# Kernel tuning notes

Hardware: AMD Instinct MI355X
Metric: run time of the kernel (lower is better)

## Reference

```python
import jax, jax.numpy as jnp
import numpy as np

B, T = 128, 512
V, E, U, K = 50000, 100, 128, 32


def _lstm(x, Wk, Wr, b):
    # x: [B, T, D] -> [B, T, U], Keras LSTM gate order i,f,g,o
    Bd = x.shape[0]
    Ud = Wr.shape[0]
    xs = jnp.swapaxes(x, 0, 1)  # [T, B, D]

    def step(carry, xt):
        h, c = carry
        z = xt @ Wk + h @ Wr + b
        i, f, g, o = jnp.split(z, 4, axis=-1)
        c = jax.nn.sigmoid(f) * c + jax.nn.sigmoid(i) * jnp.tanh(g)
        h = jax.nn.sigmoid(o) * jnp.tanh(c)
        return (h, c), h

    init = (jnp.zeros((Bd, Ud), x.dtype), jnp.zeros((Bd, Ud), x.dtype))
    _, hs = jax.lax.scan(step, init, xs)
    return jnp.swapaxes(hs, 0, 1)


def _crf_logZ(em, trans):
    # em: [B, T, K] emissions; trans: [K, K]. Forward algorithm log-partition.
    alpha0 = em[:, 0]  # [B, K]
    es = jnp.swapaxes(em[:, 1:], 0, 1)  # [T-1, B, K]

    def step(alpha, et):
        # alpha[b, i] + trans[i, j] -> logsumexp over i, plus emission
        alpha = jax.nn.logsumexp(alpha[:, :, None] + trans[None], axis=1) + et
        return alpha, None

    alphaT, _ = jax.lax.scan(step, alpha0, es)
    return jax.nn.logsumexp(alphaT, axis=-1)  # [B]


def setup_inputs() -> dict:
    key = jax.random.key(0)
    ks = jax.random.split(key, 11)
    s = 0.1
    return {
        "tokens": jax.random.randint(ks[0], (B, T), 0, V, dtype=jnp.int32),
        "emb": jax.random.normal(ks[1], (V, E), jnp.float32) * s,
        "Wk_f": jax.random.normal(ks[2], (E, 4 * U), jnp.float32) * s,
        "Wr_f": jax.random.normal(ks[3], (U, 4 * U), jnp.float32) * s,
        "b_f": jnp.zeros((4 * U,), jnp.float32),
        "Wk_b": jax.random.normal(ks[4], (E, 4 * U), jnp.float32) * s,
        "Wr_b": jax.random.normal(ks[5], (U, 4 * U), jnp.float32) * s,
        "b_b": jnp.zeros((4 * U,), jnp.float32),
        "crf_kernel": jax.random.normal(ks[6], (2 * U, K), jnp.float32) * s,
        "crf_bias": jnp.zeros((K,), jnp.float32),
        "trans": jax.random.normal(ks[7], (K, K), jnp.float32) * s,
    }


def reference(tokens, emb, Wk_f, Wr_f, b_f, Wk_b, Wr_b, b_b, crf_kernel, crf_bias, trans):
    x = emb[tokens]  # [B, T, E]
    h_f = _lstm(x, Wk_f, Wr_f, b_f)
    h_b = _lstm(x[:, ::-1], Wk_b, Wr_b, b_b)[:, ::-1]
    h = jnp.concatenate([h_f, h_b], axis=-1)  # [B, T, 2U] (dropout = identity at inference)
    em = h @ crf_kernel + crf_bias  # [B, T, K] CRF emission potentials
    return _crf_logZ(em, trans)  # [B] log-partition via CRF forward DP
```

## Files before the change

### kernel.cpp

```cpp
#include <hip/hip_runtime.h>
#include <hip/hip_bf16.h>

#define B_  128
#define T_  512
#define E_  100
#define U_  128
#define K_  32
#define G4  512
#define KP  128
#define GRP 8

typedef _Float16 h2_t __attribute__((ext_vector_type(2)));
typedef _Float16 f16x8 __attribute__((ext_vector_type(8)));
typedef __fp16   h2raw_t __attribute__((ext_vector_type(2)));
typedef short    bf16x8 __attribute__((ext_vector_type(8)));
typedef float    f32x4  __attribute__((ext_vector_type(4)));

__device__ __forceinline__ h2_t pk2(float a, float b) {
    h2raw_t r = __builtin_amdgcn_cvt_pkrtz(a, b);
    union { h2raw_t r; h2_t h; } u; u.r = r; return u.h;
}
__device__ __forceinline__ int h2_as_int(h2_t v) { union { h2_t h; int i; } u; u.h = v; return u.i; }

#if __has_builtin(__builtin_amdgcn_rcpf)
__device__ __forceinline__ float rcp_f(float x) { return __builtin_amdgcn_rcpf(x); }
#else
__device__ __forceinline__ float rcp_f(float x) { return 1.f / x; }
#endif

__device__ __forceinline__ unsigned short bf16_bits(float v) {
    __hip_bfloat16 b = __float2bfloat16(v);
    union { __hip_bfloat16 b; unsigned short s; } u; u.b = b; return u.s;
}

__global__ __launch_bounds__(128) void pack_b_kernel(
    const float* __restrict__ Wk_f, const float* __restrict__ Wk_b,
    __hip_bfloat16* __restrict__ Bb)
{
    const int n = blockIdx.x;
    const int k = threadIdx.x;
    float v = 0.f;
    if (k < E_) v = (n < 512) ? Wk_f[k * 512 + n] : Wk_b[k * 512 + (n - 512)];
    Bb[n * KP + k] = __float2bfloat16(v);
}

__global__ __launch_bounds__(256, 2) void xk_mfma_kernel(
    const int* __restrict__ tokens, const float* __restrict__ emb,
    const __hip_bfloat16* __restrict__ Bb,
    const float* __restrict__ b_f, const float* __restrict__ b_b,
    __hip_bfloat16* __restrict__ xk_f, __hip_bfloat16* __restrict__ xk_b)
{
    const int r0   = blockIdx.x * 32;
    const int tid  = threadIdx.x;
    const int wv   = tid >> 6;
    const int lane = tid & 63;
    const int quad = lane >> 4;
    const int l16  = lane & 15;

    __shared__ __align__(16) float C_lds[32][268];
    unsigned short* A_st = (unsigned short*)&C_lds[0][0];

    for (int idx = tid; idx < 32 * 64; idx += 256) {
        int r = idx >> 6, kk = idx & 63;
        unsigned int w = 0;
        if (kk < 50) {
            float2 v = *(const float2*)(emb +
                (long long)tokens[r0 + r] * E_ + 2 * kk);
            w = ((unsigned int)bf16_bits(v.y) << 16) | bf16_bits(v.x);
        }
        *(unsigned int*)&A_st[r * 136 + 2 * kk] = w;
    }
    __syncthreads();

    bf16x8 af[2][4];
    #pragma unroll
    for (int mt = 0; mt < 2; ++mt)
        #pragma unroll
        for (int kc = 0; kc < 4; ++kc)
            af[mt][kc] = *(const bf16x8*)&A_st[(mt * 16 + l16) * 136 +
                                               kc * 32 + quad * 8];
    __syncthreads();

    const unsigned short* Bu = (const unsigned short*)Bb;

    for (int ng = 0; ng < 4; ++ng) {
        const int n0 = ng * 256;

        bf16x8 bfr[4][4];
        #pragma unroll
        for (int nt = 0; nt < 4; ++nt)
            #pragma unroll
            for (int kc = 0; kc < 4; ++kc)
                bfr[nt][kc] = *(const bf16x8*)(Bu +
                    (n0 + wv * 64 + nt * 16 + l16) * KP + kc * 32 + quad * 8);

        f32x4 acc[2][4];
        #pragma unroll
        for (int mt = 0; mt < 2; ++mt)
            #pragma unroll
            for (int nt = 0; nt < 4; ++nt)
                acc[mt][nt] = (f32x4){0.f, 0.f, 0.f, 0.f};

        #pragma unroll
        for (int mt = 0; mt < 2; ++mt)
            #pragma unroll
            for (int nt = 0; nt < 4; ++nt)
                #pragma unroll
                for (int kc = 0; kc < 4; ++kc)
                    acc[mt][nt] = __builtin_amdgcn_mfma_f32_16x16x32_bf16(
                        af[mt][kc], bfr[nt][kc], acc[mt][nt], 0, 0, 0);

        #pragma unroll
        for (int mt = 0; mt < 2; ++mt)
            #pragma unroll
            for (int nt = 0; nt < 4; ++nt)
                #pragma unroll
                for (int v = 0; v < 4; ++v)
                    C_lds[mt * 16 + quad * 4 + v][wv * 64 + nt * 16 + l16] =
                        acc[mt][nt][v];
        __syncthreads();

        const float* bias = (n0 < 512) ? b_f : b_b;
        __hip_bfloat16* outp = (n0 < 512) ? xk_f : xk_b;
        const int nbase = n0 & 511;
        for (int idx = tid; idx < 32 * 128; idx += 256) {
            int r = idx >> 7, cc = (idx & 127) * 2;
            float v0 = C_lds[r][cc]     + bias[nbase + cc];
            float v1 = C_lds[r][cc + 1] + bias[nbase + cc + 1];
            unsigned int w = ((unsigned int)bf16_bits(v1) << 16) | bf16_bits(v0);
            *(unsigned int*)(outp + (long long)(r0 + r) * G4 + nbase + cc) = w;
        }
        __syncthreads();
    }
}

__device__ __forceinline__ float sigmoid_f(float x) {
    return rcp_f(1.f + __expf(-x));
}
__device__ __forceinline__ float tanh_f(float x) {
    return 1.f - 2.f * rcp_f(__expf(2.f * x) + 1.f);
}

__global__ __launch_bounds__(512, 1) void lstm_kernel(
    const __hip_bfloat16* __restrict__ xk_f,
    const __hip_bfloat16* __restrict__ xk_b,
    const float* __restrict__ Wr_f, const float* __restrict__ Wr_b,
    __hip_bfloat16* __restrict__ h_buf)
{
    const int bid  = blockIdx.x;
    const int dir  = bid >> 7;
    const int b    = bid & 127;
    const int tid  = threadIdx.x;
    const int w    = tid >> 6;
    const int lane = tid & 63;
    const int quad = lane >> 4;
    const int l16  = lane & 15;

    const float* Wr = dir ? Wr_b : Wr_f;
    const __hip_bfloat16* xk = dir ? xk_b : xk_f;

    union uf16 { f16x8 v; h2_t p[4]; uint4 u; };
    f16x8 wb[4][4];
    #pragma unroll
    for (int tt = 0; tt < 4; ++tt) {
        const int col = 64 * w + 16 * tt + l16;
        #pragma unroll
        for (int kc = 0; kc < 4; ++kc) {
            const int k0 = kc * 32 + quad * 8;
            uf16 u;
            #pragma unroll
            for (int jj = 0; jj < 4; ++jj)
                u.p[jj] = pk2(Wr[(k0 + 2 * jj)     * G4 + col],
                              Wr[(k0 + 2 * jj + 1) * G4 + col]);
            wb[tt][kc] = u.v;
        }
    }

    __shared__ __align__(16) unsigned int hpl[64];
    __shared__ float zl[G4];
    if (tid < 64) hpl[tid] = 0;
    float c = 0.f;
    __syncthreads();

    const long long rowbase = (long long)b * T_;
    const __hip_bfloat16* xkq = xk + rowbase * G4 + tid;

    float xk_cur[GRP][4];
    #pragma unroll
    for (int d = 0; d < GRP; ++d) {
        int t = dir ? (T_ - 1 - d) : d;
        #pragma unroll
        for (int g = 0; g < 4; ++g)
            xk_cur[d][g] = (tid < U_)
                ? __bfloat162float(xkq[(long long)t * G4 + g * 128]) : 0.f;
    }
    unsigned int hpack[GRP];
    #pragma unroll
    for (int d = 0; d < GRP; ++d) hpack[d] = 0;

    for (int g = 0; g < T_ / GRP; ++g) {
        float xk_nxt[GRP][4];
        #pragma unroll
        for (int d = 0; d < GRP; ++d)
            #pragma unroll
            for (int gg = 0; gg < 4; ++gg) xk_nxt[d][gg] = 0.f;
        if (tid < U_ && g + 1 < T_ / GRP) {
            #pragma unroll
            for (int d = 0; d < GRP; ++d) {
                int s = (g + 1) * GRP + d;
                int t = dir ? (T_ - 1 - s) : s;
                #pragma unroll
                for (int gg = 0; gg < 4; ++gg)
                    xk_nxt[d][gg] =
                        __bfloat162float(xkq[(long long)t * G4 + gg * 128]);
            }
        }

        #pragma unroll
        for (int d = 0; d < GRP; ++d) {
            uf16 afr[4];
            #pragma unroll
            for (int kc = 0; kc < 4; ++kc)
                afr[kc].u = *(const uint4*)&hpl[kc * 16 + quad * 4];

            f32x4 acc[4];
            #pragma unroll
            for (int tt = 0; tt < 4; ++tt)
                acc[tt] = (f32x4){0.f, 0.f, 0.f, 0.f};
            #pragma unroll
            for (int tt = 0; tt < 4; ++tt)
                #pragma unroll
                for (int kc = 0; kc < 4; ++kc)
                    acc[tt] = __builtin_amdgcn_mfma_f32_16x16x32_f16(
                        afr[kc].v, wb[tt][kc], acc[tt], 0, 0, 0);

            float zv = (quad == 0) ? acc[0][0]
                     : (quad == 1) ? acc[1][0]
                     : (quad == 2) ? acc[2][0] : acc[3][0];
            zl[64 * w + lane] = zv;
            __syncthreads();

            if (tid < U_) {
                float zi = zl[tid]           + xk_cur[d][0];
                float zf = zl[U_ + tid]      + xk_cur[d][1];
                float zg = zl[2 * U_ + tid]  + xk_cur[d][2];
                float zo = zl[3 * U_ + tid]  + xk_cur[d][3];
                c = sigmoid_f(zf) * c + sigmoid_f(zi) * tanh_f(zg);
                float h = sigmoid_f(zo) * tanh_f(c);
                float hn = __shfl_down(h, 1, 64);
                if (!(tid & 1)) {
                    hpl[tid >> 1] = (unsigned int)h2_as_int(pk2(h, hn));
                    hpack[d] = ((unsigned int)bf16_bits(hn) << 16) | bf16_bits(h);
                }
            }
            __syncthreads();
        }

        if (tid < U_ && !(tid & 1)) {
            #pragma unroll
            for (int d = 0; d < GRP; ++d) {
                int s = g * GRP + d;
                int t = dir ? (T_ - 1 - s) : s;
                *(unsigned int*)(h_buf + (rowbase + t) * 256 + dir * U_ + tid) =
                    hpack[d];
            }
        }

        #pragma unroll
        for (int d = 0; d < GRP; ++d)
            #pragma unroll
            for (int gg = 0; gg < 4; ++gg) xk_cur[d][gg] = xk_nxt[d][gg];
    }
}

__global__ __launch_bounds__(256) void em_kernel(
    const __hip_bfloat16* __restrict__ h_buf,
    const float* __restrict__ ck, const float* __restrict__ cb,
    float* __restrict__ em)
{
    const int tid  = threadIdx.x;
    const int part = tid >> 5;
    const int k    = tid & 31;

    float ckr[32];
    #pragma unroll
    for (int i = 0; i < 32; ++i)
        ckr[i] = ck[(part * 32 + i) * K_ + k];
    const float cbk = cb[k];

    __shared__ float h_l[8][256];
    __shared__ float part_l[8][8][K_];

    const int r0 = blockIdx.x * 64;

    for (int round = 0; round < 8; ++round) {
        const int rbase = r0 + round * 8;
        #pragma unroll
        for (int j = 0; j < 8; ++j)
            h_l[j][tid] = __bfloat162float(h_buf[(long long)(rbase + j) * 256 + tid]);
        __syncthreads();

        #pragma unroll
        for (int j = 0; j < 8; ++j) {
            float pp = 0.f;
            #pragma unroll
            for (int i = 0; i < 32; ++i)
                pp = fmaf(h_l[j][part * 32 + i], ckr[i], pp);
            part_l[j][part][k] = pp;
        }
        __syncthreads();

        {
            int j2 = tid >> 5;
            float e = cbk;
            #pragma unroll
            for (int pq = 0; pq < 8; ++pq) e += part_l[j2][pq][k];
            em[(long long)(rbase + j2) * K_ + k] = e;
        }
        __syncthreads();
    }
}

#define PF_ 8
__global__ __launch_bounds__(64) void crf_kernel(
    const float* __restrict__ em,
    const float* __restrict__ trans,
    float* __restrict__ out)
{
    const int b    = blockIdx.x;
    const int lane = threadIdx.x;
    const int k    = lane & 31;
    const int half = lane >> 5;

    float etr[16];
    #pragma unroll
    for (int i = 0; i < 16; ++i)
        etr[i] = __expf(trans[(half * 16 + i) * K_ + k]);

    const float* em_b = em + (long long)b * T_ * K_;

    float ep[PF_];
    #pragma unroll
    for (int d = 0; d < PF_; ++d)
        ep[d] = em_b[d * K_ + k];

    float w = 0.f;
    float L = 0.f;
    for (int tb = 0; tb < T_; tb += PF_) {
        float en[PF_];
        if (tb + PF_ < T_) {
            #pragma unroll
            for (int d = 0; d < PF_; ++d)
                en[d] = em_b[(tb + PF_ + d) * K_ + k];
        } else {
            #pragma unroll
            for (int d = 0; d < PF_; ++d) en[d] = 0.f;
        }

        float eem[PF_];
        #pragma unroll
        for (int d = 0; d < PF_; ++d) eem[d] = __expf(ep[d]);

        #pragma unroll
        for (int d = 0; d < PF_; ++d) {
            if (tb + d == 0) {
                w = eem[d];
            } else {
                float acc = 0.f;
                #pragma unroll
                for (int i = 0; i < 16; ++i) {
                    float wv = __shfl(w, half * 16 + i, 64);
                    acc = fmaf(wv, etr[i], acc);
                }
                acc += __shfl_xor(acc, 32, 64);
                w = acc * eem[d];
            }
        }

        {
            float w0 = __shfl(w, 0, 64);
            w *= rcp_f(w0);
            L += __logf(w0);
        }

        #pragma unroll
        for (int d = 0; d < PF_; ++d) ep[d] = en[d];
    }

    float s = w;
    #pragma unroll
    for (int d = 1; d < 32; d <<= 1)
        s += __shfl_xor(s, d, 64);
    if (lane == 0) out[b] = L + __logf(s);
}

extern "C" void kernel_launch(void* const* d_in, const int* in_sizes, int n_in,
                              void* d_out, int out_size, void* d_ws, size_t ws_size,
                              hipStream_t stream)
{
    const int*   tokens = (const int*)  d_in[0];
    const float* emb    = (const float*)d_in[1];
    const float* Wk_f   = (const float*)d_in[2];
    const float* Wr_f   = (const float*)d_in[3];
    const float* b_f    = (const float*)d_in[4];
    const float* Wk_b   = (const float*)d_in[5];
    const float* Wr_b   = (const float*)d_in[6];
    const float* b_b    = (const float*)d_in[7];
    const float* ck     = (const float*)d_in[8];
    const float* cb     = (const float*)d_in[9];
    const float* trans  = (const float*)d_in[10];
    float* out = (float*)d_out;

    const long long ROWS = (long long)B_ * T_;
    __hip_bfloat16* xk_f  = (__hip_bfloat16*)d_ws;
    __hip_bfloat16* xk_b  = xk_f + ROWS * G4;
    __hip_bfloat16* h_buf = xk_b + ROWS * G4;
    __hip_bfloat16* Bb    = h_buf;
    float* em = (float*)d_ws;

    hipLaunchKernelGGL(pack_b_kernel, dim3(1024), dim3(128), 0, stream,
                       Wk_f, Wk_b, Bb);
    hipLaunchKernelGGL(xk_mfma_kernel, dim3((int)(ROWS / 32)), dim3(256), 0,
                       stream, tokens, emb, Bb, b_f, b_b, xk_f, xk_b);
    hipLaunchKernelGGL(lstm_kernel, dim3(256), dim3(512), 0, stream,
                       xk_f, xk_b, Wr_f, Wr_b, h_buf);
    hipLaunchKernelGGL(em_kernel, dim3((int)(ROWS / 64)), dim3(256), 0, stream,
                       h_buf, ck, cb, em);
    hipLaunchKernelGGL(crf_kernel, dim3(B_), dim3(64), 0, stream,
                       em, trans, out);
}
```

Baseline: 630.8 us.

## Project the embedding table once and gather projected rows per token in LSTM

Instead of gathering embeddings per token and projecting all 65536 token rows, the projection now runs over the 50000-row vocabulary table, giving a [V,1024] bf16 table. The LSTM kernel gathers projected rows by token id, prefetching token ids two groups ahead. This cuts projection rows slightly but turns contiguous xk reads into random gathers from a roughly 100MB table. The workspace layout is reorganised to fit the larger table.

```diff
diff --git a/kernel.cpp b/kernel.cpp
--- a/kernel.cpp
+++ b/kernel.cpp
@@ -3,6 +3,8 @@
 
 #define B_  128
 #define T_  512
+#define V_  50000
+#define VP  50016
 #define E_  100
 #define U_  128
 #define K_  32
@@ -44,11 +46,11 @@
     Bb[n * KP + k] = __float2bfloat16(v);
 }
 
-__global__ __launch_bounds__(256, 2) void xk_mfma_kernel(
-    const int* __restrict__ tokens, const float* __restrict__ emb,
+__global__ __launch_bounds__(256, 2) void proj_mfma_kernel(
+    const float* __restrict__ emb,
     const __hip_bfloat16* __restrict__ Bb,
     const float* __restrict__ b_f, const float* __restrict__ b_b,
-    __hip_bfloat16* __restrict__ xk_f, __hip_bfloat16* __restrict__ xk_b)
+    __hip_bfloat16* __restrict__ proj)
 {
     const int r0   = blockIdx.x * 32;
     const int tid  = threadIdx.x;
@@ -62,10 +64,10 @@
 
     for (int idx = tid; idx < 32 * 64; idx += 256) {
         int r = idx >> 6, kk = idx & 63;
+        int vr = r0 + r; if (vr >= V_) vr = V_ - 1;
         unsigned int w = 0;
         if (kk < 50) {
-            float2 v = *(const float2*)(emb +
-                (long long)tokens[r0 + r] * E_ + 2 * kk);
+            float2 v = *(const float2*)(emb + (long long)vr * E_ + 2 * kk);
             w = ((unsigned int)bf16_bits(v.y) << 16) | bf16_bits(v.x);
         }
         *(unsigned int*)&A_st[r * 136 + 2 * kk] = w;
@@ -121,14 +123,13 @@
         __syncthreads();
 
         const float* bias = (n0 < 512) ? b_f : b_b;
-        __hip_bfloat16* outp = (n0 < 512) ? xk_f : xk_b;
         const int nbase = n0 & 511;
         for (int idx = tid; idx < 32 * 128; idx += 256) {
             int r = idx >> 7, cc = (idx & 127) * 2;
             float v0 = C_lds[r][cc]     + bias[nbase + cc];
             float v1 = C_lds[r][cc + 1] + bias[nbase + cc + 1];
             unsigned int w = ((unsigned int)bf16_bits(v1) << 16) | bf16_bits(v0);
-            *(unsigned int*)(outp + (long long)(r0 + r) * G4 + nbase + cc) = w;
+            *(unsigned int*)(proj + (long long)(r0 + r) * 1024 + n0 + cc) = w;
         }
         __syncthreads();
     }
@@ -142,8 +143,8 @@
 }
 
 __global__ __launch_bounds__(512, 1) void lstm_kernel(
-    const __hip_bfloat16* __restrict__ xk_f,
-    const __hip_bfloat16* __restrict__ xk_b,
+    const __hip_bfloat16* __restrict__ proj,
+    const int* __restrict__ tokens,
     const float* __restrict__ Wr_f, const float* __restrict__ Wr_b,
     __hip_bfloat16* __restrict__ h_buf)
 {
@@ -157,7 +158,6 @@
     const int l16  = lane & 15;
 
     const float* Wr = dir ? Wr_b : Wr_f;
-    const __hip_bfloat16* xk = dir ? xk_b : xk_f;
 
     union uf16 { f16x8 v; h2_t p[4]; uint4 u; };
     f16x8 wb[4][4];
@@ -182,18 +182,28 @@
     float c = 0.f;
     __syncthreads();
 
+    const int tbase = b * T_;
     const long long rowbase = (long long)b * T_;
-    const __hip_bfloat16* xkq = xk + rowbase * G4 + tid;
+    const __hip_bfloat16* pr = proj + dir * 512 + tid;
+
+    int tok_cur[GRP], tok_nxt[GRP];
+    #pragma unroll
+    for (int d = 0; d < GRP; ++d) {
+        int t0 = dir ? (T_ - 1 - d) : d;
+        tok_cur[d] = tokens[tbase + t0];
+        int t1 = dir ? (T_ - 1 - (GRP + d)) : (GRP + d);
+        tok_nxt[d] = tokens[tbase + t1];
+    }
 
     float xk_cur[GRP][4];
     #pragma unroll
-    for (int d = 0; d < GRP; ++d) {
-        int t = dir ? (T_ - 1 - d) : d;
+    for (int d = 0; d < GRP; ++d)
         #pragma unroll
         for (int g = 0; g < 4; ++g)
             xk_cur[d][g] = (tid < U_)
-                ? __bfloat162float(xkq[(long long)t * G4 + g * 128]) : 0.f;
-    }
+                ? __bfloat162float(pr[(long long)tok_cur[d] * 1024 + g * 128])
+                : 0.f;
+
     unsigned int hpack[GRP];
     #pragma unroll
     for (int d = 0; d < GRP; ++d) hpack[d] = 0;
@@ -206,13 +216,21 @@
             for (int gg = 0; gg < 4; ++gg) xk_nxt[d][gg] = 0.f;
         if (tid < U_ && g + 1 < T_ / GRP) {
             #pragma unroll
-            for (int d = 0; d < GRP; ++d) {
-                int s = (g + 1) * GRP + d;
-                int t = dir ? (T_ - 1 - s) : s;
+            for (int d = 0; d < GRP; ++d)
                 #pragma unroll
                 for (int gg = 0; gg < 4; ++gg)
-                    xk_nxt[d][gg] =
-                        __bfloat162float(xkq[(long long)t * G4 + gg * 128]);
+                    xk_nxt[d][gg] = __bfloat162float(
+                        pr[(long long)tok_nxt[d] * 1024 + gg * 128]);
+        }
+        int tok_n2[GRP];
+        #pragma unroll
+        for (int d = 0; d < GRP; ++d) tok_n2[d] = 0;
+        if (g + 2 < T_ / GRP) {
+            #pragma unroll
+            for (int d = 0; d < GRP; ++d) {
+                int s = (g + 2) * GRP + d;
+                int t = dir ? (T_ - 1 - s) : s;
+                tok_n2[d] = tokens[tbase + t];
             }
         }
 
@@ -267,9 +285,11 @@
         }
 
         #pragma unroll
-        for (int d = 0; d < GRP; ++d)
+        for (int d = 0; d < GRP; ++d) {
             #pragma unroll
             for (int gg = 0; gg < 4; ++gg) xk_cur[d][gg] = xk_nxt[d][gg];
+            tok_nxt[d] = tok_n2[d];
+        }
     }
 }
 
@@ -412,18 +432,17 @@
     float* out = (float*)d_out;
 
     const long long ROWS = (long long)B_ * T_;
-    __hip_bfloat16* xk_f  = (__hip_bfloat16*)d_ws;
-    __hip_bfloat16* xk_b  = xk_f + ROWS * G4;
-    __hip_bfloat16* h_buf = xk_b + ROWS * G4;
-    __hip_bfloat16* Bb    = h_buf;
-    float* em = (float*)d_ws;
+    __hip_bfloat16* proj  = (__hip_bfloat16*)d_ws;
+    __hip_bfloat16* h_buf = proj + (long long)VP * 1024;
+    float* em = (float*)(h_buf + ROWS * 256);
+    __hip_bfloat16* Bb = (__hip_bfloat16*)(em + ROWS * K_);
 
     hipLaunchKernelGGL(pack_b_kernel, dim3(1024), dim3(128), 0, stream,
                        Wk_f, Wk_b, Bb);
-    hipLaunchKernelGGL(xk_mfma_kernel, dim3((int)(ROWS / 32)), dim3(256), 0,
-                       stream, tokens, emb, Bb, b_f, b_b, xk_f, xk_b);
+    hipLaunchKernelGGL(proj_mfma_kernel, dim3(VP / 32), dim3(256), 0, stream,
+                       emb, Bb, b_f, b_b, proj);
     hipLaunchKernelGGL(lstm_kernel, dim3(256), dim3(512), 0, stream,
-                       xk_f, xk_b, Wr_f, Wr_b, h_buf);
+                       proj, tokens, Wr_f, Wr_b, h_buf);
     hipLaunchKernelGGL(em_kernel, dim3((int)(ROWS / 64)), dim3(256), 0, stream,
                        h_buf, ck, cb, em);
     hipLaunchKernelGGL(crf_kernel, dim3(B_), dim3(64), 0, stream,
```

New measurement: 627.2 us. Within noise of the previous version (-0.6%).
